# Kernel optimization log

Hardware: AMD Instinct MI355X
Metric: run time of the kernel (lower is better)

The kernel has to match this reference:

```python
import jax, jax.numpy as jnp
import numpy as np

N_EMBD = 1024
N_HEAD = 16
B, T = 4, 2048
EPS = 1e-5


def setup_inputs() -> dict:
    key = jax.random.key(0)
    ks = jax.random.split(key, 12)
    s = 0.02
    d, dff = N_EMBD, 4 * N_EMBD
    return {
        "x": jax.random.normal(ks[0], (B, T, d), dtype=jnp.float32),
        "ln1_w": jnp.ones((d,), jnp.float32),
        "ln1_b": jnp.zeros((d,), jnp.float32),
        "ln2_w": jnp.ones((d,), jnp.float32),
        "ln2_b": jnp.zeros((d,), jnp.float32),
        "w_attn": jax.random.normal(ks[1], (d, 3 * d), jnp.float32) * s,
        "b_attn": jnp.zeros((3 * d,), jnp.float32),
        "w_proj": jax.random.normal(ks[2], (d, d), jnp.float32) * s,
        "b_proj": jnp.zeros((d,), jnp.float32),
        "w_fc": jax.random.normal(ks[3], (d, dff), jnp.float32) * s,
        "b_fc": jnp.zeros((dff,), jnp.float32),
        "w_fc2": jax.random.normal(ks[4], (dff, d), jnp.float32) * s,
        "b_fc2": jnp.zeros((d,), jnp.float32),
    }


def _layernorm(x, w, b):
    mu = jnp.mean(x, axis=-1, keepdims=True)
    var = jnp.mean(jnp.square(x - mu), axis=-1, keepdims=True)
    return (x - mu) * jax.lax.rsqrt(var + EPS) * w + b


def reference(x, ln1_w, ln1_b, ln2_w, ln2_b, w_attn, b_attn, w_proj, b_proj,
              w_fc, b_fc, w_fc2, b_fc2):
    Bx, Tx, C = x.shape
    hd = C // N_HEAD
    # --- attention branch ---
    h = _layernorm(x, ln1_w, ln1_b)
    qkv = h @ w_attn + b_attn  # [B,T,3C]
    q, k, v = jnp.split(qkv, 3, axis=-1)
    q = q.reshape(Bx, Tx, N_HEAD, hd).transpose(0, 2, 1, 3)  # [B,H,T,hd]
    k = k.reshape(Bx, Tx, N_HEAD, hd).transpose(0, 2, 1, 3)
    v = v.reshape(Bx, Tx, N_HEAD, hd).transpose(0, 2, 1, 3)
    att = jnp.einsum("bhqd,bhkd->bhqk", q, k) * (1.0 / np.sqrt(hd))
    causal = jnp.tril(jnp.ones((Tx, Tx), dtype=bool))
    att = jnp.where(causal[None, None], att, -jnp.inf)
    att = jax.nn.softmax(att, axis=-1)
    y = jnp.einsum("bhqk,bhkd->bhqd", att, v)
    y = y.transpose(0, 2, 1, 3).reshape(Bx, Tx, C)
    x = x + (y @ w_proj + b_proj)
    # --- mlp branch ---
    h2 = _layernorm(x, ln2_w, ln2_b)
    m = jax.nn.gelu(h2 @ w_fc + b_fc, approximate=False)
    x = x + (m @ w_fc2 + b_fc2)
    return x
```

## Files before the change

kernel.cpp:

```cpp
#include <hip/hip_runtime.h>
#include <hip/hip_bf16.h>
#include <math.h>

typedef __bf16 bf16;
typedef __bf16 bf16x4 __attribute__((ext_vector_type(4)));
typedef __bf16 bf16x8 __attribute__((ext_vector_type(8)));
typedef float f32x4 __attribute__((ext_vector_type(4)));

__device__ __forceinline__ void gload_lds16(const bf16* g, bf16* l) {
  __builtin_amdgcn_global_load_lds(
      (const __attribute__((address_space(1))) void*)g,
      (__attribute__((address_space(3))) void*)l, 16, 0, 0);
}

#define MF(a, b, c) __builtin_amdgcn_mfma_f32_16x16x32_bf16((a), (b), (c), 0, 0, 0)
#define VM2_BAR()  asm volatile("s_waitcnt vmcnt(2)\ns_barrier" ::: "memory")
#define VM0_BAR()  asm volatile("s_waitcnt vmcnt(0)\ns_barrier" ::: "memory")

template <int EPI>
__global__ __launch_bounds__(512, 4)
void gemmk(const bf16* __restrict__ A, const bf16* __restrict__ BT,
           const float* __restrict__ bias, const float* __restrict__ res,
           void* __restrict__ Cout, int M, int N, int K)
{
  __shared__ alignas(16) bf16 lsA[2][8192];
  __shared__ alignas(16) bf16 lsB[2][8192];

  int nbn = N >> 7;
  int nwg = (M >> 7) * nbn;
  int bid = blockIdx.x;
  int cpx = nwg >> 3;
  int wg  = (bid & 7) * cpx + (bid >> 3);
  int m0 = (wg / nbn) << 7;
  int n0 = (wg % nbn) << 7;

  int t = threadIdx.x;
  int l = t & 63, w = t >> 6;
  int gm = w >> 2;
  int gn = w & 3;
  int lr = l & 15, lg = l >> 4;

  int nt = K >> 6;

  const bf16* Ag = A  + (size_t)m0 * K;
  const bf16* Bg = BT + (size_t)n0 * K;

  int swz0 = (lg ^ (lr & 7)) << 3;
  int swz1 = swz0 ^ 32;
  int aBase = (gm * 64 + lr) << 6;
  int bBase = (gn * 32 + lr) << 6;

  int srow = t >> 3;
  int g = (t & 7) ^ (srow & 7);
  const bf16* sA0 = Ag + (size_t)srow * K + g * 8;
  const bf16* sA1 = Ag + (size_t)(64 + srow) * K + g * 8;
  const bf16* sB0 = Bg + (size_t)srow * K + g * 8;
  const bf16* sB1 = Bg + (size_t)(64 + srow) * K + g * 8;
  int dstE = t * 8;

  f32x4 acc[4][2];
  f32x4 zero = {0.f, 0.f, 0.f, 0.f};
#pragma unroll
  for (int mi = 0; mi < 4; ++mi)
#pragma unroll
    for (int ni = 0; ni < 2; ++ni) acc[mi][ni] = zero;

  gload_lds16(sA0, &lsA[0][dstE]);
  gload_lds16(sA1, &lsA[0][4096 + dstE]);
  gload_lds16(sB0, &lsB[0][dstE]);
  gload_lds16(sB1, &lsB[0][4096 + dstE]);

  bf16x8 af[4][2], bf[2][2];

  for (int T = 0; T < nt; ++T) {
    int c = T & 1, d = c ^ 1;
    bool st = (T + 1 < nt);
    int k64 = (T + 1) << 6;

    VM2_BAR();
#pragma unroll
    for (int mi = 0; mi < 4; ++mi) {
      af[mi][0] = *(const bf16x8*)(&lsA[c][0] + aBase + mi * 1024 + swz0);
      af[mi][1] = *(const bf16x8*)(&lsA[c][0] + aBase + mi * 1024 + swz1);
    }
    if (st) {
      gload_lds16(sA0 + k64, &lsA[d][dstE]);
      gload_lds16(sA1 + k64, &lsA[d][4096 + dstE]);
    }

    if (st) VM2_BAR(); else VM0_BAR();
#pragma unroll
    for (int ni = 0; ni < 2; ++ni) {
      bf[ni][0] = *(const bf16x8*)(&lsB[c][0] + bBase + ni * 1024 + swz0);
      bf[ni][1] = *(const bf16x8*)(&lsB[c][0] + bBase + ni * 1024 + swz1);
    }
    if (st) {
      gload_lds16(sB0 + k64, &lsB[d][dstE]);
      gload_lds16(sB1 + k64, &lsB[d][4096 + dstE]);
    }
    __builtin_amdgcn_s_setprio(1);
#pragma unroll
    for (int mi = 0; mi < 4; ++mi)
#pragma unroll
      for (int ni = 0; ni < 2; ++ni)
#pragma unroll
        for (int kk = 0; kk < 2; ++kk)
          acc[mi][ni] = MF(af[mi][kk], bf[ni][kk], acc[mi][ni]);
    __builtin_amdgcn_s_setprio(0);
  }

  const float SCLQ = 0.18033688011112042f;
  bf16* Pb = (bf16*)Cout;
#pragma unroll
  for (int mi = 0; mi < 4; ++mi) {
    int row = m0 + gm * 64 + mi * 16 + lg * 4;
#pragma unroll
    for (int ni = 0; ni < 2; ++ni) {
      int col = n0 + gn * 32 + ni * 16 + lr;
      float bv = bias[col];
      f32x4 a = acc[mi][ni];
#pragma unroll
      for (int r = 0; r < 4; ++r) {
        float v = a[r] + bv;
        size_t idx = (size_t)(row + r) * N + col;
        if (EPI == 0)      Pb[idx] = (bf16)v;
        else if (EPI == 1) ((float*)Cout)[idx] = v + res[idx];
        else if (EPI == 2) Pb[idx] = (bf16)(0.5f * v * (1.f + erff(v * 0.70710678118654752f)));
        else if (EPI == 4) Pb[idx] = (bf16)((col < 1024) ? v * SCLQ : v);
      }
    }
  }
}

__global__ __launch_bounds__(256)
void ln_bf16(const float* __restrict__ x, const float* __restrict__ w,
             const float* __restrict__ b, bf16* __restrict__ out)
{
  int row = blockIdx.x;
  int t = threadIdx.x;
  float4 v = ((const float4*)(x + (size_t)row * 1024))[t];
  float s  = v.x + v.y + v.z + v.w;
  float sq = v.x * v.x + v.y * v.y + v.z * v.z + v.w * v.w;
#pragma unroll
  for (int off = 32; off >= 1; off >>= 1) {
    s  += __shfl_xor(s, off);
    sq += __shfl_xor(sq, off);
  }
  __shared__ float ps[4], pq[4];
  if ((t & 63) == 0) { ps[t >> 6] = s; pq[t >> 6] = sq; }
  __syncthreads();
  s  = ps[0] + ps[1] + ps[2] + ps[3];
  sq = pq[0] + pq[1] + pq[2] + pq[3];
  float mu  = s * (1.f / 1024.f);
  float var = sq * (1.f / 1024.f) - mu * mu;
  float rstd = rsqrtf(var + 1e-5f);
  float4 wv = ((const float4*)w)[t];
  float4 bv = ((const float4*)b)[t];
  size_t o0 = (size_t)row * 1024 + t * 4;
  out[o0 + 0] = (bf16)((v.x - mu) * rstd * wv.x + bv.x);
  out[o0 + 1] = (bf16)((v.y - mu) * rstd * wv.y + bv.y);
  out[o0 + 2] = (bf16)((v.z - mu) * rstd * wv.z + bv.z);
  out[o0 + 3] = (bf16)((v.w - mu) * rstd * wv.w + bv.w);
}

__global__ __launch_bounds__(256)
void transpose_cast(const float* __restrict__ W, bf16* __restrict__ WT, int K, int N)
{
  __shared__ float tile[32][33];
  int bk = blockIdx.x * 32, bn = blockIdx.y * 32;
  int tx = threadIdx.x & 31, ty = threadIdx.x >> 5;
#pragma unroll
  for (int i = ty; i < 32; i += 8)
    tile[i][tx] = W[(size_t)(bk + i) * N + bn + tx];
  __syncthreads();
#pragma unroll
  for (int i = ty; i < 32; i += 8)
    WT[(size_t)(bn + i) * K + bk + tx] = (bf16)tile[tx][i];
}

__global__ __launch_bounds__(256)
void vtrans(const bf16* __restrict__ qkv, bf16* __restrict__ vt)
{
  __shared__ alignas(16) bf16 tile[64 * 64];
  int bh = blockIdx.x;
  int b = bh >> 4, h = bh & 15;
  int t0 = blockIdx.y * 64;
  int t = threadIdx.x;
#pragma unroll
  for (int i = 0; i < 2; ++i) {
    int c = i * 256 + t;
    int tt = c >> 3, d8 = c & 7;
    bf16x8 v = *(const bf16x8*)(qkv + (size_t)(b * 2048 + t0 + tt) * 3072 + 2048 + h * 64 + d8 * 8);
    *(bf16x8*)&tile[(tt * 8 + (d8 ^ (tt >> 3))) * 8] = v;
  }
  __syncthreads();
#pragma unroll
  for (int i = 0; i < 2; ++i) {
    int c = i * 256 + t;
    int d = c >> 3, tt8 = c & 7;
    bf16x8 o;
#pragma unroll
    for (int j = 0; j < 8; ++j) {
      int row = tt8 * 8 + j;
      o[j] = tile[(row * 8 + ((d >> 3) ^ (row >> 3))) * 8 + (d & 7)];
    }
    *(bf16x8*)(vt + (size_t)(bh * 64 + d) * 2048 + t0 + tt8 * 8) = o;
  }
}

__global__ __launch_bounds__(512)
void attn_flash(const bf16* __restrict__ qkv, const bf16* __restrict__ vt,
                bf16* __restrict__ y)
{
  __shared__ alignas(16) bf16 lk[2][4096];
  __shared__ alignas(16) bf16 lv[2][4096];
  __shared__ alignas(16) bf16 lp[8][16 * 64];

  int bid = blockIdx.x;
  int bh = bid & 63;
  int qb = 15 - (bid >> 6);
  int b = bh >> 4, h = bh & 15;
  int t = threadIdx.x;
  int w = t >> 6, l = t & 63;
  int lr = l & 15, lg = l >> 4;
  int q0 = qb * 128;
  int qw = q0 + w * 16;
  const size_t RS = 3072;

  const bf16* qbase = qkv + (size_t)(b * 2048) * RS + h * 64;
  const bf16* kbase = qkv + (size_t)(b * 2048) * RS + 1024 + h * 64;
  const bf16* vtb   = vt + (size_t)(bh * 64) * 2048;

  bf16x8 qf[2];
#pragma unroll
  for (int kk = 0; kk < 2; ++kk)
    qf[kk] = *(const bf16x8*)(qbase + (size_t)(qw + lr) * RS + kk * 32 + lg * 8);

  int row = t >> 3, c8 = t & 7;
  int sc8 = c8 ^ (row & 7);
  const bf16* pK = kbase + (size_t)row * RS + sc8 * 8;
  const bf16* pV = vtb + (size_t)row * 2048 + sc8 * 8;
  int dst = t * 8;

  f32x4 zero = {0.f, 0.f, 0.f, 0.f};
  f32x4 o[4];
#pragma unroll
  for (int ni = 0; ni < 4; ++ni) o[ni] = zero;
  float lo[4] = {0.f, 0.f, 0.f, 0.f};

  int nkb = 2 * qb + 2;
  gload_lds16(pK, &lk[0][dst]);
  gload_lds16(pV, &lv[0][dst]);

  for (int kb = 0; kb < nkb; ++kb) {
    int cur = kb & 1;
    int k0 = kb * 64;
    VM0_BAR();
    if (kb + 1 < nkb) {
      pK += 64 * RS;
      pV += 64;
      gload_lds16(pK, &lk[cur ^ 1][dst]);
      gload_lds16(pV, &lv[cur ^ 1][dst]);
    }

    f32x4 s[4];
#pragma unroll
    for (int j = 0; j < 4; ++j) s[j] = zero;
#pragma unroll
    for (int kk = 0; kk < 2; ++kk)
#pragma unroll
      for (int j = 0; j < 4; ++j) {
        int krow = j * 16 + lr;
        bf16x8 kf = *(const bf16x8*)&lk[cur][krow * 64 + (((4 * kk + lg) ^ (krow & 7)) * 8)];
        s[j] = MF(qf[kk], kf, s[j]);
      }

    bool needmask = (k0 + 63 > qw);
    float p[4][4];
#pragma unroll
    for (int r = 0; r < 4; ++r) {
      int tq = qw + lg * 4 + r;
#pragma unroll
      for (int j = 0; j < 4; ++j) {
        float v = s[j][r];
        if (needmask && (k0 + j * 16 + lr > tq)) v = -1e30f;
        p[j][r] = exp2f(v);
      }
      lo[r] += (p[0][r] + p[1][r]) + (p[2][r] + p[3][r]);
    }

#pragma unroll
    for (int r = 0; r < 4; ++r) {
      int qr = lg * 4 + r;
#pragma unroll
      for (int j = 0; j < 4; ++j) {
        int ch = (2 * j + (lr >> 3)) ^ (qr & 7);
        lp[w][qr * 64 + ch * 8 + (lr & 7)] = (bf16)p[j][r];
      }
    }
    bf16x8 pa[2];
#pragma unroll
    for (int kf = 0; kf < 2; ++kf)
      pa[kf] = *(const bf16x8*)&lp[w][lr * 64 + (((4 * kf + lg) ^ (lr & 7)) * 8)];

#pragma unroll
    for (int ni = 0; ni < 4; ++ni)
#pragma unroll
      for (int kf = 0; kf < 2; ++kf) {
        int d = ni * 16 + lr;
        bf16x8 vf = *(const bf16x8*)&lv[cur][d * 64 + (((4 * kf + lg) ^ (d & 7)) * 8)];
        o[ni] = MF(pa[kf], vf, o[ni]);
      }
  }

#pragma unroll
  for (int r = 0; r < 4; ++r) {
#pragma unroll
    for (int off = 1; off < 16; off <<= 1) lo[r] += __shfl_xor(lo[r], off);
    lo[r] = 1.f / lo[r];
  }
#pragma unroll
  for (int ni = 0; ni < 4; ++ni)
#pragma unroll
    for (int r = 0; r < 4; ++r) {
      int tq = qw + lg * 4 + r;
      y[(size_t)(b * 2048 + tq) * 1024 + h * 64 + ni * 16 + lr] = (bf16)(o[ni][r] * lo[r]);
    }
}

extern "C" void kernel_launch(void* const* d_in, const int* in_sizes, int n_in,
                              void* d_out, int out_size, void* d_ws, size_t ws_size,
                              hipStream_t stream) {
  (void)in_sizes; (void)n_in; (void)out_size; (void)ws_size;
  const float* x      = (const float*)d_in[0];
  const float* ln1w   = (const float*)d_in[1];
  const float* ln1b   = (const float*)d_in[2];
  const float* ln2w   = (const float*)d_in[3];
  const float* ln2b   = (const float*)d_in[4];
  const float* w_attn = (const float*)d_in[5];
  const float* b_attn = (const float*)d_in[6];
  const float* w_proj = (const float*)d_in[7];
  const float* b_proj = (const float*)d_in[8];
  const float* w_fc   = (const float*)d_in[9];
  const float* b_fc   = (const float*)d_in[10];
  const float* w_fc2  = (const float*)d_in[11];
  const float* b_fc2  = (const float*)d_in[12];
  float* out = (float*)d_out;

  char* p = (char*)d_ws;
  bf16*  h     = (bf16*)p;  p += (size_t)8192 * 1024 * 2;
  bf16*  qkv   = (bf16*)p;
  bf16*  mbuf  = (bf16*)p;  p += (size_t)8192 * 3072 * 2;
  bf16*  ybuf  = (bf16*)p;  p += (size_t)8192 * 1024 * 2;
  float* x1    = (float*)p; p += (size_t)8192 * 1024 * 4;
  bf16*  wqkvT = (bf16*)p;  p += (size_t)3072 * 1024 * 2;
  bf16*  wprojT= (bf16*)p;  p += (size_t)1024 * 1024 * 2;
  bf16*  wfcT  = (bf16*)p;  p += (size_t)4096 * 1024 * 2;
  bf16*  wfc2T = (bf16*)p;  p += (size_t)1024 * 4096 * 2;
  bf16*  vt    = (bf16*)x1;

  transpose_cast<<<dim3(1024 / 32, 3072 / 32), 256, 0, stream>>>(w_attn, wqkvT, 1024, 3072);
  transpose_cast<<<dim3(1024 / 32, 1024 / 32), 256, 0, stream>>>(w_proj, wprojT, 1024, 1024);
  transpose_cast<<<dim3(1024 / 32, 4096 / 32), 256, 0, stream>>>(w_fc,   wfcT,  1024, 4096);
  transpose_cast<<<dim3(4096 / 32, 1024 / 32), 256, 0, stream>>>(w_fc2,  wfc2T, 4096, 1024);

  ln_bf16<<<8192, 256, 0, stream>>>(x, ln1w, ln1b, h);
  gemmk<4><<<1536, 512, 0, stream>>>(h, wqkvT, b_attn, nullptr, qkv, 8192, 3072, 1024);
  vtrans<<<dim3(64, 32), 256, 0, stream>>>(qkv, vt);
  attn_flash<<<1024, 512, 0, stream>>>(qkv, vt, ybuf);
  gemmk<1><<<512, 512, 0, stream>>>(ybuf, wprojT, b_proj, x, x1, 8192, 1024, 1024);
  ln_bf16<<<8192, 256, 0, stream>>>(x1, ln2w, ln2b, h);
  gemmk<2><<<2048, 512, 0, stream>>>(h, wfcT, b_fc, nullptr, mbuf, 8192, 4096, 1024);
  gemmk<1><<<512, 512, 0, stream>>>(mbuf, wfc2T, b_fc2, x1, out, 8192, 1024, 4096);
}
```

Before: 394.8 us.

## Use 4-wave GEMM workgroups with 64x64 per-wave tiles

```diff
diff --git a/kernel.cpp b/kernel.cpp
--- a/kernel.cpp
+++ b/kernel.cpp
@@ -14,12 +14,12 @@
 }
 
 #define MF(a, b, c) __builtin_amdgcn_mfma_f32_16x16x32_bf16((a), (b), (c), 0, 0, 0)
-#define VM2_BAR()  asm volatile("s_waitcnt vmcnt(2)\ns_barrier" ::: "memory")
+#define VM4_BAR()  asm volatile("s_waitcnt vmcnt(4)\ns_barrier" ::: "memory")
 #define VM0_BAR()  asm volatile("s_waitcnt vmcnt(0)\ns_barrier" ::: "memory")
 
 template <int EPI>
-__global__ __launch_bounds__(512, 4)
-void gemmk(const bf16* __restrict__ A, const bf16* __restrict__ BT,
+__global__ __launch_bounds__(256, 2)
+void gemmw(const bf16* __restrict__ A, const bf16* __restrict__ BT,
            const float* __restrict__ bias, const float* __restrict__ res,
            void* __restrict__ Cout, int M, int N, int K)
 {
@@ -36,8 +36,8 @@
 
   int t = threadIdx.x;
   int l = t & 63, w = t >> 6;
-  int gm = w >> 2;
-  int gn = w & 3;
+  int gm = w >> 1;
+  int gn = w & 1;
   int lr = l & 15, lg = l >> 4;
 
   int nt = K >> 6;
@@ -48,61 +48,70 @@
   int swz0 = (lg ^ (lr & 7)) << 3;
   int swz1 = swz0 ^ 32;
   int aBase = (gm * 64 + lr) << 6;
-  int bBase = (gn * 32 + lr) << 6;
-
-  int srow = t >> 3;
-  int g = (t & 7) ^ (srow & 7);
-  const bf16* sA0 = Ag + (size_t)srow * K + g * 8;
-  const bf16* sA1 = Ag + (size_t)(64 + srow) * K + g * 8;
-  const bf16* sB0 = Bg + (size_t)srow * K + g * 8;
-  const bf16* sB1 = Bg + (size_t)(64 + srow) * K + g * 8;
-  int dstE = t * 8;
-
-  f32x4 acc[4][2];
+  int bBase = (gn * 64 + lr) << 6;
+
+  const bf16* srcA[2]; const bf16* srcB[2]; int dstE[2];
+#pragma unroll
+  for (int j = 0; j < 2; ++j) {
+    int ci = j * 256 + t;
+    int row = ci >> 3;
+    int g = (ci & 7) ^ (row & 7);
+    srcA[j] = Ag + (size_t)row * K + g * 8;
+    srcB[j] = Bg + (size_t)row * K + g * 8;
+    dstE[j] = ci * 8;
+  }
+  size_t h64 = (size_t)64 * K;
+
+#define STAGE_A(kofs, db) do { \
+  gload_lds16(srcA[0] + (kofs), &lsA[db][dstE[0]]); \
+  gload_lds16(srcA[1] + (kofs), &lsA[db][dstE[1]]); \
+  gload_lds16(srcA[0] + h64 + (kofs), &lsA[db][4096 + dstE[0]]); \
+  gload_lds16(srcA[1] + h64 + (kofs), &lsA[db][4096 + dstE[1]]); \
+} while (0)
+#define STAGE_B(kofs, db) do { \
+  gload_lds16(srcB[0] + (kofs), &lsB[db][dstE[0]]); \
+  gload_lds16(srcB[1] + (kofs), &lsB[db][dstE[1]]); \
+  gload_lds16(srcB[0] + h64 + (kofs), &lsB[db][4096 + dstE[0]]); \
+  gload_lds16(srcB[1] + h64 + (kofs), &lsB[db][4096 + dstE[1]]); \
+} while (0)
+
+  f32x4 acc[4][4];
   f32x4 zero = {0.f, 0.f, 0.f, 0.f};
 #pragma unroll
   for (int mi = 0; mi < 4; ++mi)
 #pragma unroll
-    for (int ni = 0; ni < 2; ++ni) acc[mi][ni] = zero;
-
-  gload_lds16(sA0, &lsA[0][dstE]);
-  gload_lds16(sA1, &lsA[0][4096 + dstE]);
-  gload_lds16(sB0, &lsB[0][dstE]);
-  gload_lds16(sB1, &lsB[0][4096 + dstE]);
-
-  bf16x8 af[4][2], bf[2][2];
+    for (int ni = 0; ni < 4; ++ni) acc[mi][ni] = zero;
+
+  STAGE_A(0, 0);
+  STAGE_B(0, 0);
+
+  bf16x8 af[4][2], bf[4][2];
 
   for (int T = 0; T < nt; ++T) {
     int c = T & 1, d = c ^ 1;
     bool st = (T + 1 < nt);
     int k64 = (T + 1) << 6;
 
-    VM2_BAR();
+    VM4_BAR();
 #pragma unroll
     for (int mi = 0; mi < 4; ++mi) {
       af[mi][0] = *(const bf16x8*)(&lsA[c][0] + aBase + mi * 1024 + swz0);
       af[mi][1] = *(const bf16x8*)(&lsA[c][0] + aBase + mi * 1024 + swz1);
     }
-    if (st) {
-      gload_lds16(sA0 + k64, &lsA[d][dstE]);
-      gload_lds16(sA1 + k64, &lsA[d][4096 + dstE]);
-    }
-
-    if (st) VM2_BAR(); else VM0_BAR();
-#pragma unroll
-    for (int ni = 0; ni < 2; ++ni) {
+    if (st) STAGE_A(k64, d);
+
+    if (st) VM4_BAR(); else VM0_BAR();
+#pragma unroll
+    for (int ni = 0; ni < 4; ++ni) {
       bf[ni][0] = *(const bf16x8*)(&lsB[c][0] + bBase + ni * 1024 + swz0);
       bf[ni][1] = *(const bf16x8*)(&lsB[c][0] + bBase + ni * 1024 + swz1);
     }
-    if (st) {
-      gload_lds16(sB0 + k64, &lsB[d][dstE]);
-      gload_lds16(sB1 + k64, &lsB[d][4096 + dstE]);
-    }
+    if (st) STAGE_B(k64, d);
     __builtin_amdgcn_s_setprio(1);
 #pragma unroll
     for (int mi = 0; mi < 4; ++mi)
 #pragma unroll
-      for (int ni = 0; ni < 2; ++ni)
+      for (int ni = 0; ni < 4; ++ni)
 #pragma unroll
         for (int kk = 0; kk < 2; ++kk)
           acc[mi][ni] = MF(af[mi][kk], bf[ni][kk], acc[mi][ni]);
@@ -115,8 +124,8 @@
   for (int mi = 0; mi < 4; ++mi) {
     int row = m0 + gm * 64 + mi * 16 + lg * 4;
 #pragma unroll
-    for (int ni = 0; ni < 2; ++ni) {
-      int col = n0 + gn * 32 + ni * 16 + lr;
+    for (int ni = 0; ni < 4; ++ni) {
+      int col = n0 + gn * 64 + ni * 16 + lr;
       float bv = bias[col];
       f32x4 a = acc[mi][ni];
 #pragma unroll
@@ -130,6 +139,8 @@
       }
     }
   }
+#undef STAGE_A
+#undef STAGE_B
 }
 
 __global__ __launch_bounds__(256)
@@ -365,11 +376,11 @@
   transpose_cast<<<dim3(4096 / 32, 1024 / 32), 256, 0, stream>>>(w_fc2,  wfc2T, 4096, 1024);
 
   ln_bf16<<<8192, 256, 0, stream>>>(x, ln1w, ln1b, h);
-  gemmk<4><<<1536, 512, 0, stream>>>(h, wqkvT, b_attn, nullptr, qkv, 8192, 3072, 1024);
+  gemmw<4><<<1536, 256, 0, stream>>>(h, wqkvT, b_attn, nullptr, qkv, 8192, 3072, 1024);
   vtrans<<<dim3(64, 32), 256, 0, stream>>>(qkv, vt);
   attn_flash<<<1024, 512, 0, stream>>>(qkv, vt, ybuf);
-  gemmk<1><<<512, 512, 0, stream>>>(ybuf, wprojT, b_proj, x, x1, 8192, 1024, 1024);
+  gemmw<1><<<512, 256, 0, stream>>>(ybuf, wprojT, b_proj, x, x1, 8192, 1024, 1024);
   ln_bf16<<<8192, 256, 0, stream>>>(x1, ln2w, ln2b, h);
-  gemmk<2><<<2048, 512, 0, stream>>>(h, wfcT, b_fc, nullptr, mbuf, 8192, 4096, 1024);
-  gemmk<1><<<512, 512, 0, stream>>>(mbuf, wfc2T, b_fc2, x1, out, 8192, 1024, 4096);
-}
+  gemmw<2><<<2048, 256, 0, stream>>>(h, wfcT, b_fc, nullptr, mbuf, 8192, 4096, 1024);
+  gemmw<1><<<512, 256, 0, stream>>>(mbuf, wfc2T, b_fc2, x1, out, 8192, 1024, 4096);
+}
```

After: 402.8 us. 2.0% more time.

## Pass attention probabilities through lane shuffles instead of LDS, skip fully masked key blocks

Applied to the files above, without the earlier changes.

```diff
diff --git a/kernel.cpp b/kernel.cpp
--- a/kernel.cpp
+++ b/kernel.cpp
@@ -6,11 +6,19 @@
 typedef __bf16 bf16x4 __attribute__((ext_vector_type(4)));
 typedef __bf16 bf16x8 __attribute__((ext_vector_type(8)));
 typedef float f32x4 __attribute__((ext_vector_type(4)));
+typedef unsigned int u32;
+typedef unsigned int u32x4 __attribute__((ext_vector_type(4)));
 
 __device__ __forceinline__ void gload_lds16(const bf16* g, bf16* l) {
   __builtin_amdgcn_global_load_lds(
       (const __attribute__((address_space(1))) void*)g,
       (__attribute__((address_space(3))) void*)l, 16, 0, 0);
+}
+
+__device__ __forceinline__ u32 pk2(float a, float b) {
+  union { bf16 h; unsigned short u; } x, y;
+  x.h = (bf16)a; y.h = (bf16)b;
+  return (u32)x.u | ((u32)y.u << 16);
 }
 
 #define MF(a, b, c) __builtin_amdgcn_mfma_f32_16x16x32_bf16((a), (b), (c), 0, 0, 0)
@@ -214,7 +222,6 @@
 {
   __shared__ alignas(16) bf16 lk[2][4096];
   __shared__ alignas(16) bf16 lv[2][4096];
-  __shared__ alignas(16) bf16 lp[8][16 * 64];
 
   int bid = blockIdx.x;
   int bh = bid & 63;
@@ -246,7 +253,11 @@
   f32x4 o[4];
 #pragma unroll
   for (int ni = 0; ni < 4; ++ni) o[ni] = zero;
-  float lo[4] = {0.f, 0.f, 0.f, 0.f};
+  float lo = 0.f;
+
+  int srcA = lr + ((lg & 1) << 5);
+  int srcB = srcA + 16;
+  int jhalf = lg >> 1;
 
   int nkb = 2 * qb + 2;
   gload_lds16(pK, &lk[0][dst]);
@@ -262,6 +273,7 @@
       gload_lds16(pK, &lk[cur ^ 1][dst]);
       gload_lds16(pV, &lv[cur ^ 1][dst]);
     }
+    if (k0 > qw + 15) continue;
 
     f32x4 s[4];
 #pragma unroll
@@ -272,59 +284,61 @@
       for (int j = 0; j < 4; ++j) {
         int krow = j * 16 + lr;
         bf16x8 kf = *(const bf16x8*)&lk[cur][krow * 64 + (((4 * kk + lg) ^ (krow & 7)) * 8)];
-        s[j] = MF(qf[kk], kf, s[j]);
+        s[j] = MF(kf, qf[kk], s[j]);
       }
 
     bool needmask = (k0 + 63 > qw);
-    float p[4][4];
+    u32 packL[4], packH[4];
+#pragma unroll
+    for (int j = 0; j < 4; ++j) {
+      int kbase_j = k0 + j * 16 + lg * 4;
+      int tq = qw + lr;
+      float v0 = s[j][0], v1 = s[j][1], v2 = s[j][2], v3 = s[j][3];
+      if (needmask) {
+        if (kbase_j + 0 > tq) v0 = -1e30f;
+        if (kbase_j + 1 > tq) v1 = -1e30f;
+        if (kbase_j + 2 > tq) v2 = -1e30f;
+        if (kbase_j + 3 > tq) v3 = -1e30f;
+      }
+      float p0 = exp2f(v0), p1 = exp2f(v1), p2 = exp2f(v2), p3 = exp2f(v3);
+      lo += (p0 + p1) + (p2 + p3);
+      packL[j] = pk2(p0, p1);
+      packH[j] = pk2(p2, p3);
+    }
+
+#pragma unroll
+    for (int kf = 0; kf < 2; ++kf) {
+      u32 la0 = __shfl(packL[2 * kf], srcA), la1 = __shfl(packL[2 * kf + 1], srcA);
+      u32 ha0 = __shfl(packH[2 * kf], srcA), ha1 = __shfl(packH[2 * kf + 1], srcA);
+      u32 lb0 = __shfl(packL[2 * kf], srcB), lb1 = __shfl(packL[2 * kf + 1], srcB);
+      u32 hb0 = __shfl(packH[2 * kf], srcB), hb1 = __shfl(packH[2 * kf + 1], srcB);
+      u32x4 pa32;
+      pa32[0] = jhalf ? la1 : la0;
+      pa32[1] = jhalf ? ha1 : ha0;
+      pa32[2] = jhalf ? lb1 : lb0;
+      pa32[3] = jhalf ? hb1 : hb0;
+      bf16x8 pa = __builtin_bit_cast(bf16x8, pa32);
+#pragma unroll
+      for (int ni = 0; ni < 4; ++ni) {
+        int d = ni * 16 + lr;
+        bf16x8 vf = *(const bf16x8*)&lv[cur][d * 64 + (((4 * kf + lg) ^ (d & 7)) * 8)];
+        o[ni] = MF(pa, vf, o[ni]);
+      }
+    }
+  }
+
+  lo += __shfl_xor(lo, 16);
+  lo += __shfl_xor(lo, 32);
+  float inv[4];
+#pragma unroll
+  for (int r = 0; r < 4; ++r)
+    inv[r] = 1.f / __shfl(lo, (lg << 4) | (lg * 4 + r));
+#pragma unroll
+  for (int ni = 0; ni < 4; ++ni)
 #pragma unroll
     for (int r = 0; r < 4; ++r) {
       int tq = qw + lg * 4 + r;
-#pragma unroll
-      for (int j = 0; j < 4; ++j) {
-        float v = s[j][r];
-        if (needmask && (k0 + j * 16 + lr > tq)) v = -1e30f;
-        p[j][r] = exp2f(v);
-      }
-      lo[r] += (p[0][r] + p[1][r]) + (p[2][r] + p[3][r]);
-    }
-
-#pragma unroll
-    for (int r = 0; r < 4; ++r) {
-      int qr = lg * 4 + r;
-#pragma unroll
-      for (int j = 0; j < 4; ++j) {
-        int ch = (2 * j + (lr >> 3)) ^ (qr & 7);
-        lp[w][qr * 64 + ch * 8 + (lr & 7)] = (bf16)p[j][r];
-      }
-    }
-    bf16x8 pa[2];
-#pragma unroll
-    for (int kf = 0; kf < 2; ++kf)
-      pa[kf] = *(const bf16x8*)&lp[w][lr * 64 + (((4 * kf + lg) ^ (lr & 7)) * 8)];
-
-#pragma unroll
-    for (int ni = 0; ni < 4; ++ni)
-#pragma unroll
-      for (int kf = 0; kf < 2; ++kf) {
-        int d = ni * 16 + lr;
-        bf16x8 vf = *(const bf16x8*)&lv[cur][d * 64 + (((4 * kf + lg) ^ (d & 7)) * 8)];
-        o[ni] = MF(pa[kf], vf, o[ni]);
-      }
-  }
-
-#pragma unroll
-  for (int r = 0; r < 4; ++r) {
-#pragma unroll
-    for (int off = 1; off < 16; off <<= 1) lo[r] += __shfl_xor(lo[r], off);
-    lo[r] = 1.f / lo[r];
-  }
-#pragma unroll
-  for (int ni = 0; ni < 4; ++ni)
-#pragma unroll
-    for (int r = 0; r < 4; ++r) {
-      int tq = qw + lg * 4 + r;
-      y[(size_t)(b * 2048 + tq) * 1024 + h * 64 + ni * 16 + lr] = (bf16)(o[ni][r] * lo[r]);
+      y[(size_t)(b * 2048 + tq) * 1024 + h * 64 + ni * 16 + lr] = (bf16)(o[ni][r] * inv[r]);
     }
 }
 
```

After: 388.4 us. Within noise of the previous version (-1.6%).
